# Performance work log

Measured on AMD Instinct MI355X. Metric: run time of the kernel, lower is better.

The kernel has to match this reference:

```python
import jax, jax.numpy as jnp
import numpy as np

B, T, D, H, E, DLAT = 4, 2048, 512, 8, 32, 64
DH = D // H  # head_dim = 64


def rmsnorm(x, gamma, eps=1e-6):
    norm = jnp.sqrt(jnp.mean(jnp.square(x), axis=-1, keepdims=True) + eps)
    return gamma * (x / norm)


def apply_rope(x):
    # x: (B, T, H, Dh); rotate-half style RoPE over last dim
    _, t, _, d = x.shape
    inv_freq = 1.0 / (10000.0 ** (jnp.arange(0, d, 2, dtype=jnp.float32) / d))
    freqs = jnp.outer(jnp.arange(t, dtype=jnp.float32), inv_freq)  # (T, d/2)
    sin = jnp.sin(freqs)[None, :, None, :]
    cos = jnp.cos(freqs)[None, :, None, :]
    x1, x2 = jnp.split(x, 2, axis=-1)
    return jnp.concatenate([x1 * cos - x2 * sin, x1 * sin + x2 * cos], axis=-1)


def setup_inputs() -> dict:
    key = jax.random.key(0)
    ks = jax.random.split(key, 8)
    s = lambda fan_in: 1.0 / np.sqrt(fan_in)
    return {
        "x": jax.random.normal(ks[0], (B, T, D), jnp.float32),
        "gamma1": jnp.ones((D,), jnp.float32),
        "gamma2": jnp.ones((D,), jnp.float32),
        "wq": jax.random.normal(ks[1], (D, D), jnp.float32) * s(D),
        "bq": jnp.zeros((D,), jnp.float32),
        "wkd": jax.random.normal(ks[2], (D, DLAT), jnp.float32) * s(D),
        "bkd": jnp.zeros((DLAT,), jnp.float32),
        "wku": jax.random.normal(ks[3], (DLAT, 2 * D), jnp.float32) * s(DLAT),
        "bku": jnp.zeros((2 * D,), jnp.float32),
        "wo": jax.random.normal(ks[4], (D, D), jnp.float32) * s(D),
        "bo": jnp.zeros((D,), jnp.float32),
        "wg": jax.random.normal(ks[5], (D, E), jnp.float32) * s(D),
        "bg": jnp.zeros((E,), jnp.float32),
        "expert_w": jax.random.normal(ks[6], (E, D, D), jnp.float32) * s(D),
    }


def reference(x, gamma1, gamma2, wq, bq, wkd, bkd, wku, bku, wo, bo, wg, bg, expert_w):
    b, t, d = x.shape
    # --- MLA attention branch ---
    h = rmsnorm(x, gamma1)
    q = (h @ wq + bq).reshape(b, t, H, DH)
    kv = ((h @ wkd + bkd) @ wku + bku).reshape(b, t, H, 2 * DH)
    k, v = jnp.split(kv, 2, axis=-1)
    q = apply_rope(q)
    k = apply_rope(k)
    # NOTE (faithful to source): attention is across HEADS per timestep -> (B,T,H,H)
    att = jnp.einsum("bthd,btgd->bthg", q, k) / jnp.sqrt(jnp.float32(DH))
    att = jax.nn.softmax(att, axis=-1)
    out = jnp.einsum("bthg,btgd->bthd", att, v).reshape(b, t, d)
    x = x + (out @ wo + bo)
    # --- dense soft-MoE branch ---
    h2 = rmsnorm(x, gamma2)
    gate = jax.nn.softmax(h2 @ wg + bg, axis=-1)  # (B, T, E)
    moe = jnp.einsum("btd,edf,bte->btf", h2, expert_w, gate)
    return x + moe
```

## Files before the change

### kernel.cpp

```cpp
#include <hip/hip_runtime.h>
#include <hip/hip_bf16.h>

#define B_ 4
#define T_ 2048
#define D_ 512
#define H_ 8
#define E_ 32
#define DLAT_ 64
#define DH_ 64
#define M_ (B_*T_)

typedef unsigned short u16;
typedef unsigned int u32;
typedef __bf16 bf16x8 __attribute__((ext_vector_type(8)));
typedef float f32x4 __attribute__((ext_vector_type(4)));

__device__ __forceinline__ float bf2f(u16 u) {
    union { u32 i; float f; } c; c.i = ((u32)u) << 16; return c.f;
}
__device__ __forceinline__ u16 f2bf(float f) {
    union { float f; u32 i; } c; c.f = f;
    u32 x = c.i; x += 0x7fffu + ((x >> 16) & 1u);
    return (u16)(x >> 16);
}
__device__ __forceinline__ u32 pack2(float a, float b) {
    return (u32)f2bf(a) | ((u32)f2bf(b) << 16);
}

__global__ __launch_bounds__(256) void transpose_f2b(
    const float* __restrict__ src, u16* __restrict__ dst,
    int R, int C, int dstStride, long srcBatchStride, int dstBatchOff)
{
    __shared__ float tile[32][33];
    const int z = blockIdx.z;
    const float* s = src + (long)z * srcBatchStride;
    const int c0 = blockIdx.x * 32, r0 = blockIdx.y * 32;
    const int tx = threadIdx.x, ty = threadIdx.y;
#pragma unroll
    for (int i = 0; i < 32; i += 8) {
        int r = r0 + ty + i, c = c0 + tx;
        if (r < R && c < C) tile[ty + i][tx] = s[(long)r * C + c];
    }
    __syncthreads();
#pragma unroll
    for (int i = 0; i < 32; i += 8) {
        int c = c0 + ty + i, r = r0 + tx;
        if (r < R && c < C)
            dst[(long)c * dstStride + (long)z * dstBatchOff + r] = f2bf(tile[tx][ty + i]);
    }
}

__global__ __launch_bounds__(256) void rmsnorm_k(
    const float* __restrict__ x, const float* __restrict__ gamma,
    float* __restrict__ of, u16* __restrict__ ob)
{
    const size_t row = blockIdx.x;
    const int t = threadIdx.x;
    const float* xr = x + row * D_;
    float2 v = *(const float2*)(xr + 2 * t);
    float ss = v.x * v.x + v.y * v.y;
#pragma unroll
    for (int off = 1; off < 64; off <<= 1) ss += __shfl_xor(ss, off, 64);
    __shared__ float wsum[4];
    if ((t & 63) == 0) wsum[t >> 6] = ss;
    __syncthreads();
    float tot = wsum[0] + wsum[1] + wsum[2] + wsum[3];
    float inv = rsqrtf(tot * (1.0f / D_) + 1e-6f);
    float o0 = v.x * inv * gamma[2 * t];
    float o1 = v.y * inv * gamma[2 * t + 1];
    if (of) *(float2*)(of + row * D_ + 2 * t) = make_float2(o0, o1);
    if (ob) *(u32*)(ob + row * D_ + 2 * t) = pack2(o0, o1);
}

__global__ __launch_bounds__(512, 4) void gemm8w(
    const u16* __restrict__ A, const u16* __restrict__ Bt,
    const float* __restrict__ bias, const float* __restrict__ resid,
    float* __restrict__ outF, u16* __restrict__ outB, int Ndim, int strideA, int K)
{
    __shared__ __align__(16) u16 lA[128][72];
    __shared__ __align__(16) u16 lB[128][72];
    const int t = threadIdx.x;
    const int lane = t & 63, wid = t >> 6;
    const int wr = wid >> 2, wc = wid & 3;
    const int rowBase = blockIdx.x * 128;
    const int colBase = blockIdx.y * 128;
    const int srow = t >> 3;
    const int scol = (t & 7) * 8;
    const int l15 = lane & 15;
    const int kreg = (lane >> 4) * 8;

    f32x4 acc[4][2] = {};

    for (int kb = 0; kb < K; kb += 64) {
#pragma unroll
        for (int i = 0; i < 2; ++i) {
            int r = srow + 64 * i;
            *(int4*)(&lA[r][scol]) =
                *(const int4*)(A + (size_t)(rowBase + r) * strideA + kb + scol);
            *(int4*)(&lB[r][scol]) =
                *(const int4*)(Bt + (size_t)(colBase + r) * K + kb + scol);
        }
        __syncthreads();
#pragma unroll
        for (int kk = 0; kk < 64; kk += 32) {
            const int ko = kk + kreg;
            bf16x8 af[4], bfr[2];
#pragma unroll
            for (int mi = 0; mi < 4; ++mi)
                af[mi] = *(const bf16x8*)(&lA[wr * 64 + mi * 16 + l15][ko]);
#pragma unroll
            for (int ni = 0; ni < 2; ++ni)
                bfr[ni] = *(const bf16x8*)(&lB[wc * 32 + ni * 16 + l15][ko]);
#pragma unroll
            for (int mi = 0; mi < 4; ++mi)
#pragma unroll
                for (int ni = 0; ni < 2; ++ni)
                    acc[mi][ni] = __builtin_amdgcn_mfma_f32_16x16x32_bf16(
                        af[mi], bfr[ni], acc[mi][ni], 0, 0, 0);
        }
        __syncthreads();
    }
#pragma unroll
    for (int mi = 0; mi < 4; ++mi)
#pragma unroll
        for (int ni = 0; ni < 2; ++ni)
#pragma unroll
            for (int r = 0; r < 4; ++r) {
                int grow = rowBase + wr * 64 + mi * 16 + (lane >> 4) * 4 + r;
                int gcol = colBase + wc * 32 + ni * 16 + l15;
                float v = acc[mi][ni][r];
                if (bias)  v += bias[gcol];
                if (resid) v += resid[(size_t)grow * Ndim + gcol];
                if (outF)  outF[(size_t)grow * Ndim + gcol] = v;
                if (outB)  outB[(size_t)grow * Ndim + gcol] = f2bf(v);
            }
}

#define KPS_ 4096
__global__ __launch_bounds__(512, 4) void moe256(
    const u16* __restrict__ A, const u16* __restrict__ Bt,
    const float* __restrict__ gate, const float* __restrict__ resid,
    float* __restrict__ part)
{
    __shared__ __align__(16) u16 lA[256][72];
    __shared__ __align__(16) u16 lB[128][72];
    const int t = threadIdx.x;
    const int lane = t & 63, wid = t >> 6;
    const int wr = wid >> 1, wc = wid & 1;
    const int rowBase = blockIdx.x * 256;
    const int colBase = blockIdx.y * 128;
    const int z = blockIdx.z;
    const int eBase = z * (KPS_ / 512);
    float* outF = part + (size_t)z * M_ * D_;
    const float* rz = (z == 0) ? resid : nullptr;
    const int srow = t >> 3;
    const int scol = (t & 7) * 8;
    const int l15 = lane & 15;
    const int kreg = (lane >> 4) * 8;

    f32x4 acc[4][4] = {};

    for (int ei = 0; ei < 8; ++ei) {
        const int e = eBase + ei;
        float g[4];
#pragma unroll
        for (int i = 0; i < 4; ++i)
            g[i] = gate[(size_t)(rowBase + srow + 64 * i) * E_ + e];
#pragma unroll 1
        for (int k8 = 0; k8 < 8; ++k8) {
            const int akb = k8 * 64;
            const int kb = e * 512 + akb;
#pragma unroll
            for (int i = 0; i < 4; ++i) {
                int r = srow + 64 * i;
                bf16x8 raw = *(const bf16x8*)(A + (size_t)(rowBase + r) * 512 + akb + scol);
                bf16x8 o;
#pragma unroll
                for (int j = 0; j < 8; ++j)
                    o[j] = (__bf16)((float)raw[j] * g[i]);
                *(bf16x8*)(&lA[r][scol]) = o;
            }
#pragma unroll
            for (int i = 0; i < 2; ++i) {
                int r = srow + 64 * i;
                *(int4*)(&lB[r][scol]) =
                    *(const int4*)(Bt + (size_t)(colBase + r) * (E_ * 512) + kb + scol);
            }
            __syncthreads();
#pragma unroll
            for (int kk = 0; kk < 64; kk += 32) {
                const int ko = kk + kreg;
                bf16x8 af[4], bfr[4];
#pragma unroll
                for (int mi = 0; mi < 4; ++mi)
                    af[mi] = *(const bf16x8*)(&lA[wr * 64 + mi * 16 + l15][ko]);
#pragma unroll
                for (int ni = 0; ni < 4; ++ni)
                    bfr[ni] = *(const bf16x8*)(&lB[wc * 64 + ni * 16 + l15][ko]);
#pragma unroll
                for (int mi = 0; mi < 4; ++mi)
#pragma unroll
                    for (int ni = 0; ni < 4; ++ni)
                        acc[mi][ni] = __builtin_amdgcn_mfma_f32_16x16x32_bf16(
                            af[mi], bfr[ni], acc[mi][ni], 0, 0, 0);
            }
            __syncthreads();
        }
    }
#pragma unroll
    for (int mi = 0; mi < 4; ++mi)
#pragma unroll
        for (int ni = 0; ni < 4; ++ni)
#pragma unroll
            for (int r = 0; r < 4; ++r) {
                int grow = rowBase + wr * 64 + mi * 16 + (lane >> 4) * 4 + r;
                int gcol = colBase + wc * 64 + ni * 16 + l15;
                float v = acc[mi][ni][r];
                if (rz) v += rz[(size_t)grow * D_ + gcol];
                outF[(size_t)grow * D_ + gcol] = v;
            }
}

__global__ __launch_bounds__(256) void gemm_bt(
    const u16* __restrict__ A, const u16* __restrict__ Bt,
    const float* __restrict__ bias, float* __restrict__ outF,
    u16* __restrict__ outB, int Ndim, int K)
{
    __shared__ __align__(16) u16 lA[128][72];
    __shared__ __align__(16) u16 lB[64][72];
    const int t = threadIdx.x;
    const int lane = t & 63, wid = t >> 6;
    const int rowBase = blockIdx.x * 128;
    const int colBase = blockIdx.y * 64;
    const int srow = t >> 3;
    const int skb = (t & 7) * 8;
    const int l15 = lane & 15;
    const int kreg = (lane >> 4) * 8;

    f32x4 accT[2][4] = {};

    for (int kb = 0; kb < K; kb += 64) {
#pragma unroll
        for (int i = 0; i < 4; ++i) {
            int r = srow + 32 * i;
            size_t grow = (size_t)(rowBase + r);
            *(int4*)(&lA[r][skb]) = *(const int4*)(A + grow * (size_t)K + kb + skb);
        }
#pragma unroll
        for (int i = 0; i < 2; ++i) {
            int n = srow + 32 * i;
            int gn = colBase + n;
            int4 v = {0, 0, 0, 0};
            if (gn < Ndim) v = *(const int4*)(Bt + (size_t)gn * K + kb + skb);
            *(int4*)(&lB[n][skb]) = v;
        }
        __syncthreads();
#pragma unroll
        for (int kk = 0; kk < 64; kk += 32) {
            const int ko = kk + kreg;
            bf16x8 af[2], bfr[4];
            af[0] = *(const bf16x8*)(&lA[wid * 32 + l15][ko]);
            af[1] = *(const bf16x8*)(&lA[wid * 32 + 16 + l15][ko]);
#pragma unroll
            for (int ni = 0; ni < 4; ++ni)
                bfr[ni] = *(const bf16x8*)(&lB[ni * 16 + l15][ko]);
#pragma unroll
            for (int mi = 0; mi < 2; ++mi)
#pragma unroll
                for (int ni = 0; ni < 4; ++ni)
                    accT[mi][ni] = __builtin_amdgcn_mfma_f32_16x16x32_bf16(
                        af[mi], bfr[ni], accT[mi][ni], 0, 0, 0);
        }
        __syncthreads();
    }
#pragma unroll
    for (int mi = 0; mi < 2; ++mi)
#pragma unroll
        for (int ni = 0; ni < 4; ++ni)
#pragma unroll
            for (int r = 0; r < 4; ++r) {
                int grow = rowBase + wid * 32 + mi * 16 + (lane >> 4) * 4 + r;
                int gcol = colBase + ni * 16 + l15;
                if (gcol < Ndim) {
                    float v = accT[mi][ni][r];
                    if (bias)  v += bias[gcol];
                    if (outF)  outF[(size_t)grow * Ndim + gcol] = v;
                    if (outB)  outB[(size_t)grow * Ndim + gcol] = f2bf(v);
                }
            }
}

__global__ __launch_bounds__(256) void reduce4_k(
    const float* __restrict__ p, float* __restrict__ o, int n4)
{
    int i = blockIdx.x * 256 + threadIdx.x;
    const int stride = gridDim.x * 256;
    for (; i < n4; i += stride) {
        float4 v0 = ((const float4*)p)[i];
        float4 v1 = ((const float4*)p)[i + n4];
        float4 v2 = ((const float4*)p)[i + 2 * n4];
        float4 v3 = ((const float4*)p)[i + 3 * n4];
        float4 r;
        r.x = v0.x + v1.x + v2.x + v3.x;
        r.y = v0.y + v1.y + v2.y + v3.y;
        r.z = v0.z + v1.z + v2.z + v3.z;
        r.w = v0.w + v1.w + v2.w + v3.w;
        ((float4*)o)[i] = r;
    }
}

__global__ __launch_bounds__(256) void rope_build(float2* __restrict__ tab)
{
    int i = blockIdx.x * 256 + threadIdx.x;
    int tpos = i >> 5, j = i & 31;
    float inv = exp2f(-(float)j * (13.287712379549449f / 32.0f));
    float ang = (float)tpos * inv;
    float sn, cs;
    sincosf(ang, &sn, &cs);
    tab[i] = make_float2(cs, sn);
}

__global__ __launch_bounds__(64) void attn_k(
    const float* __restrict__ q, const float* __restrict__ kv,
    const float2* __restrict__ rope, u16* __restrict__ out)
{
    const int tok = blockIdx.x;
    const int tpos = tok & (T_ - 1);
    const int l = threadIdx.x;
    __shared__ float sq[8][65], sk[8][65], sv[8][65];
    __shared__ float satt[8][9];
    const int h = l >> 3;
    const int j0 = (l & 7) * 4;
    const float* qr = q + (size_t)tok * 512;
    const float* kr = kv + (size_t)tok * 1024;
#pragma unroll
    for (int jj = 0; jj < 4; ++jj) {
        int j = j0 + jj;
        float2 cssn = rope[tpos * 32 + j];
        float cs = cssn.x, sn = cssn.y;
        float q1 = qr[h * 64 + j], q2 = qr[h * 64 + 32 + j];
        sq[h][j] = q1 * cs - q2 * sn;
        sq[h][j + 32] = q1 * sn + q2 * cs;
        float k1 = kr[h * 128 + j], k2 = kr[h * 128 + 32 + j];
        sk[h][j] = k1 * cs - k2 * sn;
        sk[h][j + 32] = k1 * sn + k2 * cs;
        sv[h][j] = kr[h * 128 + 64 + j];
        sv[h][j + 32] = kr[h * 128 + 96 + j];
    }
    __syncthreads();
    const int g = l & 7;
    float s = 0.f;
#pragma unroll 8
    for (int c = 0; c < 64; ++c) s += sq[h][c] * sk[g][c];
    s *= 0.125f;
    float m = s;
#pragma unroll
    for (int off = 4; off; off >>= 1) m = fmaxf(m, __shfl_xor(m, off, 8));
    float p = __expf(s - m);
    float den = p;
#pragma unroll
    for (int off = 4; off; off >>= 1) den += __shfl_xor(den, off, 8);
    satt[h][g] = p / den;
    __syncthreads();
    const int c8 = (l & 7) * 8;
    float o[8] = {};
#pragma unroll
    for (int gg = 0; gg < 8; ++gg) {
        float a = satt[h][gg];
#pragma unroll
        for (int i = 0; i < 8; ++i) o[i] += a * sv[gg][c8 + i];
    }
    int4 pk;
    pk.x = pack2(o[0], o[1]); pk.y = pack2(o[2], o[3]);
    pk.z = pack2(o[4], o[5]); pk.w = pack2(o[6], o[7]);
    *(int4*)(out + (size_t)tok * 512 + h * 64 + c8) = pk;
}

__global__ __launch_bounds__(256) void gate_k(
    const u16* __restrict__ h2, const float* __restrict__ wg,
    const float* __restrict__ bg, float* __restrict__ gate)
{
    __shared__ float sh[8][516];
    const int t = threadIdx.x;
    const size_t tok0 = (size_t)blockIdx.x * 8;
#pragma unroll
    for (int i = 0; i < 2; ++i) {
        int chunk = t + i * 256;
        int row = chunk >> 6;
        int c8 = (chunk & 63) * 8;
        int4 raw = *(const int4*)(h2 + (tok0 + row) * 512 + c8);
        u32 wv[4] = {(u32)raw.x, (u32)raw.y, (u32)raw.z, (u32)raw.w};
#pragma unroll
        for (int j = 0; j < 4; ++j) {
            sh[row][c8 + 2 * j] = bf2f((u16)(wv[j] & 0xffff));
            sh[row][c8 + 2 * j + 1] = bf2f((u16)(wv[j] >> 16));
        }
    }
    __syncthreads();
    const int e = t & 31;
    const int tl = t >> 5;
    float acc = bg[e];
#pragma unroll 4
    for (int d = 0; d < 512; ++d) acc += sh[tl][d] * wg[d * 32 + e];
    float m = acc;
#pragma unroll
    for (int off = 16; off; off >>= 1) m = fmaxf(m, __shfl_xor(m, off, 32));
    float p = __expf(acc - m);
    float ssum = p;
#pragma unroll
    for (int off = 16; off; off >>= 1) ssum += __shfl_xor(ssum, off, 32);
    gate[(tok0 + tl) * 32 + e] = p / ssum;
}

extern "C" void kernel_launch(void* const* d_in, const int* in_sizes, int n_in,
                              void* d_out, int out_size, void* d_ws, size_t ws_size,
                              hipStream_t stream)
{
    const float* x      = (const float*)d_in[0];
    const float* gamma1 = (const float*)d_in[1];
    const float* gamma2 = (const float*)d_in[2];
    const float* wq     = (const float*)d_in[3];
    const float* bq     = (const float*)d_in[4];
    const float* wkd    = (const float*)d_in[5];
    const float* bkd    = (const float*)d_in[6];
    const float* wku    = (const float*)d_in[7];
    const float* bku    = (const float*)d_in[8];
    const float* wo     = (const float*)d_in[9];
    const float* bo     = (const float*)d_in[10];
    const float* wg     = (const float*)d_in[11];
    const float* bg     = (const float*)d_in[12];
    const float* expw   = (const float*)d_in[13];

    char* w = (char*)d_ws;
    size_t off = 0;
    auto alloc = [&](size_t bytes) -> void* {
        void* p = w + off; off += (bytes + 255) & ~(size_t)255; return p;
    };
    u16*   h_b    = (u16*)alloc((size_t)M_ * D_ * 2);
    u16*   kd_b   = (u16*)alloc((size_t)M_ * DLAT_ * 2);
    u16*   at_b   = (u16*)alloc((size_t)M_ * D_ * 2);
    u16*   h2_b   = (u16*)alloc((size_t)M_ * D_ * 2);
    float* q_f    = (float*)alloc((size_t)M_ * D_ * 4);
    float* kv_f   = (float*)alloc((size_t)M_ * 2 * D_ * 4);
    float* pext   = (float*)alloc((size_t)M_ * D_ * 4);
    float* x1_f   = (float*)alloc((size_t)M_ * D_ * 4);
    float* gate_f = (float*)alloc((size_t)M_ * E_ * 4);
    float2* rope_t = (float2*)alloc((size_t)T_ * 32 * 8);
    u16*   wqT    = (u16*)alloc((size_t)D_ * D_ * 2);
    u16*   wkdT   = (u16*)alloc((size_t)D_ * DLAT_ * 2);
    u16*   wkuT   = (u16*)alloc((size_t)DLAT_ * 2 * D_ * 2);
    u16*   woT    = (u16*)alloc((size_t)D_ * D_ * 2);
    u16*   expT   = (u16*)alloc((size_t)E_ * D_ * D_ * 2);
    (void)ws_size; (void)in_sizes; (void)n_in; (void)out_size; (void)pext;

    float* parts = q_f;

    dim3 tb(32, 8);
    transpose_f2b<<<dim3(16, 16, 1), tb, 0, stream>>>(wq,  wqT,  512, 512, 512, 0L, 0);
    transpose_f2b<<<dim3(2, 16, 1),  tb, 0, stream>>>(wkd, wkdT, 512, 64,  512, 0L, 0);
    transpose_f2b<<<dim3(32, 2, 1),  tb, 0, stream>>>(wku, wkuT, 64, 1024, 64,  0L, 0);
    transpose_f2b<<<dim3(16, 16, 1), tb, 0, stream>>>(wo,  woT,  512, 512, 512, 0L, 0);
    transpose_f2b<<<dim3(16, 16, 32), tb, 0, stream>>>(expw, expT, 512, 512, 16384,
                                                       (long)512 * 512, 512);
    rope_build<<<(T_ * 32) / 256, 256, 0, stream>>>(rope_t);
    rmsnorm_k<<<M_, 256, 0, stream>>>(x, gamma1, nullptr, h_b);
    gemm8w<<<dim3(64, 4), 512, 0, stream>>>(h_b, wqT, bq, nullptr, q_f, nullptr,
                                            512, 512, 512);
    gemm_bt<<<dim3(64, 1), 256, 0, stream>>>(h_b, wkdT, bkd, nullptr, kd_b, 64, 512);
    gemm8w<<<dim3(64, 8), 512, 0, stream>>>(kd_b, wkuT, bku, nullptr, kv_f, nullptr,
                                            1024, 64, 64);
    attn_k<<<M_, 64, 0, stream>>>(q_f, kv_f, rope_t, at_b);
    gemm8w<<<dim3(64, 4), 512, 0, stream>>>(at_b, woT, bo, x, x1_f, nullptr,
                                            512, 512, 512);
    rmsnorm_k<<<M_, 256, 0, stream>>>(x1_f, gamma2, nullptr, h2_b);
    gate_k<<<M_ / 8, 256, 0, stream>>>(h2_b, wg, bg, gate_f);
    moe256<<<dim3(32, 4, 4), 512, 0, stream>>>(h2_b, expT, gate_f, x1_f, parts);
    reduce4_k<<<2048, 256, 0, stream>>>(parts, (float*)d_out, M_ * D_ / 4);
}
```

Measured before the change: 358.9 us.

## Double-buffer MoE GEMM with register prefetch and halve split-K partials

```diff
diff --git a/kernel.cpp b/kernel.cpp
--- a/kernel.cpp
+++ b/kernel.cpp
@@ -136,14 +136,14 @@
             }
 }
 
-#define KPS_ 4096
-__global__ __launch_bounds__(512, 4) void moe256(
+#define KPS_ 8192
+__global__ __launch_bounds__(512, 2) void moe256(
     const u16* __restrict__ A, const u16* __restrict__ Bt,
     const float* __restrict__ gate, const float* __restrict__ resid,
     float* __restrict__ part)
 {
-    __shared__ __align__(16) u16 lA[256][72];
-    __shared__ __align__(16) u16 lB[128][72];
+    __shared__ __align__(16) u16 lA[2][256][72];
+    __shared__ __align__(16) u16 lB[2][128][72];
     const int t = threadIdx.x;
     const int lane = t & 63, wid = t >> 6;
     const int wr = wid >> 1, wc = wid & 1;
@@ -157,56 +157,73 @@
     const int scol = (t & 7) * 8;
     const int l15 = lane & 15;
     const int kreg = (lane >> 4) * 8;
+    const int NT = KPS_ / 64;
 
     f32x4 acc[4][4] = {};
-
-    for (int ei = 0; ei < 8; ++ei) {
-        const int e = eBase + ei;
-        float g[4];
-#pragma unroll
-        for (int i = 0; i < 4; ++i)
-            g[i] = gate[(size_t)(rowBase + srow + 64 * i) * E_ + e];
+    int4 ra[4], rb[2];
+    float g[4];
+
+    auto issue = [&](int tt) {
+        const int e = eBase + (tt >> 3);
+        const int akb = (tt & 7) * 64;
+        const int kb = e * 512 + akb;
+#pragma unroll
+        for (int i = 0; i < 4; ++i) {
+            int r = rowBase + srow + 64 * i;
+            ra[i] = *(const int4*)(A + (size_t)r * 512 + akb + scol);
+            g[i] = gate[(size_t)r * E_ + e];
+        }
+#pragma unroll
+        for (int i = 0; i < 2; ++i)
+            rb[i] = *(const int4*)(Bt + (size_t)(colBase + srow + 64 * i) * (E_ * 512)
+                                   + kb + scol);
+    };
+    auto foldwrite = [&](int buf) {
+#pragma unroll
+        for (int i = 0; i < 4; ++i) {
+            bf16x8 raw = *(bf16x8*)&ra[i];
+            bf16x8 o;
+#pragma unroll
+            for (int j = 0; j < 8; ++j)
+                o[j] = (__bf16)((float)raw[j] * g[i]);
+            *(bf16x8*)(&lA[buf][srow + 64 * i][scol]) = o;
+        }
+#pragma unroll
+        for (int i = 0; i < 2; ++i)
+            *(int4*)(&lB[buf][srow + 64 * i][scol]) = rb[i];
+    };
+    auto compute = [&](int buf) {
+#pragma unroll
+        for (int kk = 0; kk < 64; kk += 32) {
+            const int ko = kk + kreg;
+            bf16x8 af[4], bfr[4];
+#pragma unroll
+            for (int mi = 0; mi < 4; ++mi)
+                af[mi] = *(const bf16x8*)(&lA[buf][wr * 64 + mi * 16 + l15][ko]);
+#pragma unroll
+            for (int ni = 0; ni < 4; ++ni)
+                bfr[ni] = *(const bf16x8*)(&lB[buf][wc * 64 + ni * 16 + l15][ko]);
+#pragma unroll
+            for (int mi = 0; mi < 4; ++mi)
+#pragma unroll
+                for (int ni = 0; ni < 4; ++ni)
+                    acc[mi][ni] = __builtin_amdgcn_mfma_f32_16x16x32_bf16(
+                        af[mi], bfr[ni], acc[mi][ni], 0, 0, 0);
+        }
+    };
+
+    issue(0);
+    foldwrite(0);
+    __syncthreads();
 #pragma unroll 1
-        for (int k8 = 0; k8 < 8; ++k8) {
-            const int akb = k8 * 64;
-            const int kb = e * 512 + akb;
-#pragma unroll
-            for (int i = 0; i < 4; ++i) {
-                int r = srow + 64 * i;
-                bf16x8 raw = *(const bf16x8*)(A + (size_t)(rowBase + r) * 512 + akb + scol);
-                bf16x8 o;
-#pragma unroll
-                for (int j = 0; j < 8; ++j)
-                    o[j] = (__bf16)((float)raw[j] * g[i]);
-                *(bf16x8*)(&lA[r][scol]) = o;
-            }
-#pragma unroll
-            for (int i = 0; i < 2; ++i) {
-                int r = srow + 64 * i;
-                *(int4*)(&lB[r][scol]) =
-                    *(const int4*)(Bt + (size_t)(colBase + r) * (E_ * 512) + kb + scol);
-            }
-            __syncthreads();
-#pragma unroll
-            for (int kk = 0; kk < 64; kk += 32) {
-                const int ko = kk + kreg;
-                bf16x8 af[4], bfr[4];
-#pragma unroll
-                for (int mi = 0; mi < 4; ++mi)
-                    af[mi] = *(const bf16x8*)(&lA[wr * 64 + mi * 16 + l15][ko]);
-#pragma unroll
-                for (int ni = 0; ni < 4; ++ni)
-                    bfr[ni] = *(const bf16x8*)(&lB[wc * 64 + ni * 16 + l15][ko]);
-#pragma unroll
-                for (int mi = 0; mi < 4; ++mi)
-#pragma unroll
-                    for (int ni = 0; ni < 4; ++ni)
-                        acc[mi][ni] = __builtin_amdgcn_mfma_f32_16x16x32_bf16(
-                            af[mi], bfr[ni], acc[mi][ni], 0, 0, 0);
-            }
-            __syncthreads();
-        }
-    }
+    for (int tt = 0; tt < NT - 1; ++tt) {
+        issue(tt + 1);
+        compute(tt & 1);
+        foldwrite((tt + 1) & 1);
+        __syncthreads();
+    }
+    compute((NT - 1) & 1);
+
 #pragma unroll
     for (int mi = 0; mi < 4; ++mi)
 #pragma unroll
@@ -290,7 +307,7 @@
             }
 }
 
-__global__ __launch_bounds__(256) void reduce4_k(
+__global__ __launch_bounds__(256) void reduce2_k(
     const float* __restrict__ p, float* __restrict__ o, int n4)
 {
     int i = blockIdx.x * 256 + threadIdx.x;
@@ -298,13 +315,11 @@
     for (; i < n4; i += stride) {
         float4 v0 = ((const float4*)p)[i];
         float4 v1 = ((const float4*)p)[i + n4];
-        float4 v2 = ((const float4*)p)[i + 2 * n4];
-        float4 v3 = ((const float4*)p)[i + 3 * n4];
         float4 r;
-        r.x = v0.x + v1.x + v2.x + v3.x;
-        r.y = v0.y + v1.y + v2.y + v3.y;
-        r.z = v0.z + v1.z + v2.z + v3.z;
-        r.w = v0.w + v1.w + v2.w + v3.w;
+        r.x = v0.x + v1.x;
+        r.y = v0.y + v1.y;
+        r.z = v0.z + v1.z;
+        r.w = v0.w + v1.w;
         ((float4*)o)[i] = r;
     }
 }
@@ -442,7 +457,6 @@
     u16*   h2_b   = (u16*)alloc((size_t)M_ * D_ * 2);
     float* q_f    = (float*)alloc((size_t)M_ * D_ * 4);
     float* kv_f   = (float*)alloc((size_t)M_ * 2 * D_ * 4);
-    float* pext   = (float*)alloc((size_t)M_ * D_ * 4);
     float* x1_f   = (float*)alloc((size_t)M_ * D_ * 4);
     float* gate_f = (float*)alloc((size_t)M_ * E_ * 4);
     float2* rope_t = (float2*)alloc((size_t)T_ * 32 * 8);
@@ -451,7 +465,7 @@
     u16*   wkuT   = (u16*)alloc((size_t)DLAT_ * 2 * D_ * 2);
     u16*   woT    = (u16*)alloc((size_t)D_ * D_ * 2);
     u16*   expT   = (u16*)alloc((size_t)E_ * D_ * D_ * 2);
-    (void)ws_size; (void)in_sizes; (void)n_in; (void)out_size; (void)pext;
+    (void)ws_size; (void)in_sizes; (void)n_in; (void)out_size;
 
     float* parts = q_f;
 
@@ -474,6 +488,6 @@
                                             512, 512, 512);
     rmsnorm_k<<<M_, 256, 0, stream>>>(x1_f, gamma2, nullptr, h2_b);
     gate_k<<<M_ / 8, 256, 0, stream>>>(h2_b, wg, bg, gate_f);
-    moe256<<<dim3(32, 4, 4), 512, 0, stream>>>(h2_b, expT, gate_f, x1_f, parts);
-    reduce4_k<<<2048, 256, 0, stream>>>(parts, (float*)d_out, M_ * D_ / 4);
-}
+    moe256<<<dim3(32, 4, 2), 512, 0, stream>>>(h2_b, expT, gate_f, x1_f, parts);
+    reduce2_k<<<2048, 256, 0, stream>>>(parts, (float*)d_out, M_ * D_ / 4);
+}
```

Measured after the change: 409.9 us. +14.2%, slower.
